# Optimization experiments

Measured on AMD Instinct MI355X. Metric: run time of the kernel, lower is better.

The kernel has to match this reference:

```python
import jax, jax.numpy as jnp
import numpy as np

B, S, D, H, HD, W, DFF = 2, 8192, 768, 12, 64, 256, 3072
NEG = -1e9


def ln(x, s, b, eps):
    m = jnp.mean(x, axis=-1, keepdims=True)
    v = jnp.mean((x - m) ** 2, axis=-1, keepdims=True)
    return (x - m) / jnp.sqrt(v + eps) * s + b


def band_attn(q, k, v, w):
    # q,k,v: [B,H,S,HD]; q already scaled by 1/sqrt(HD).
    b, h, s, d = q.shape
    nc = s // w  # non-overlapping query chunks of size w
    qc = q.reshape(b, h, nc, w, d)
    pad = ((0, 0), (0, 0), (w, w), (0, 0))
    kp = jnp.pad(k, pad)
    vp = jnp.pad(v, pad)
    # key chunk c covers global positions [c*w - w, c*w + 2w) -> length 3w
    idx = jnp.arange(nc)[:, None] * w + jnp.arange(3 * w)[None, :]  # [nc,3w]
    kc = kp[:, :, idx]  # [B,H,nc,3w,HD]
    vc = vp[:, :, idx]
    scores = jnp.einsum('bhcqd,bhckd->bhcqk', qc, kc)  # [B,H,nc,w,3w]
    # relative offset key-query: key global = c*w - w + j, query global = c*w + i
    rel = jnp.arange(3 * w)[None, :] - w - jnp.arange(w)[:, None]  # [w,3w]
    band = jnp.abs(rel) <= w
    kpos = jnp.arange(nc)[:, None] * w - w + jnp.arange(3 * w)[None, :]  # [nc,3w]
    valid = (kpos >= 0) & (kpos < s)
    mask = band[None, :, :] & valid[:, None, :]  # [nc,w,3w]
    scores = jnp.where(mask, scores, NEG)
    probs = jax.nn.softmax(scores, axis=-1)
    out = jnp.einsum('bhcqk,bhckd->bhcqd', probs, vc)
    return out.reshape(b, h, s, d)


def longformer_layer(hidden, pos_emb, tt_emb, emb_ln_s, emb_ln_b,
                     wq, bq, wk, bk, wv, bv, wo, bo, attn_ln_s, attn_ln_b,
                     wi, bi, wo2, bo2, out_ln_s, out_ln_b):
    # embeddings: inputs_embeds + position + token_type(0), LN eps 1e-12
    h = ln(hidden + pos_emb[None, :hidden.shape[1]] + tt_emb, emb_ln_s, emb_ln_b, 1e-12)
    def heads(x):
        return x.reshape(B, S, H, HD).transpose(0, 2, 1, 3)
    q = heads(h @ wq + bq) / jnp.sqrt(jnp.float32(HD))
    k = heads(h @ wk + bk)
    v = heads(h @ wv + bv)
    a = band_attn(q, k, v, W)  # [B,H,S,HD]
    a = a.transpose(0, 2, 1, 3).reshape(B, S, D)
    h2 = ln(h + (a @ wo + bo), attn_ln_s, attn_ln_b, 1e-12)
    inter = jax.nn.gelu(h2 @ wi + bi, approximate=False)
    return ln(h2 + (inter @ wo2 + bo2), out_ln_s, out_ln_b, 1e-12)


def setup_inputs() -> dict:
    key = jax.random.key(0)
    ks = jax.random.split(key, 16)
    wn = lambda k, shp: jax.random.normal(k, shp, jnp.float32) * 0.02
    d = {
        'src': jax.random.normal(ks[0], (B, S, D), jnp.float32),
        'pos_emb': wn(ks[1], (S, D)),
        'tt_emb': wn(ks[2], (D,)),
        'emb_ln_s': jnp.ones((D,)), 'emb_ln_b': jnp.zeros((D,)),
        'wq': wn(ks[3], (D, D)), 'bq': jnp.zeros((D,)),
        'wk': wn(ks[4], (D, D)), 'bk': jnp.zeros((D,)),
        'wv': wn(ks[5], (D, D)), 'bv': jnp.zeros((D,)),
        'wo': wn(ks[6], (D, D)), 'bo': jnp.zeros((D,)),
        'attn_ln_s': jnp.ones((D,)), 'attn_ln_b': jnp.zeros((D,)),
        'wi': wn(ks[7], (D, DFF)), 'bi': jnp.zeros((DFF,)),
        'wo2': wn(ks[8], (DFF, D)), 'bo2': jnp.zeros((D,)),
        'out_ln_s': jnp.ones((D,)), 'out_ln_b': jnp.zeros((D,)),
        'n1_s': jnp.ones((D,)), 'n1_b': jnp.zeros((D,)),
        'n2_s': jnp.ones((D,)), 'n2_b': jnp.zeros((D,)),
        'w1': wn(ks[9], (D, DFF)), 'b1': jnp.zeros((DFF,)),
        'w2': wn(ks[10], (DFF, D)), 'b2': jnp.zeros((D,)),
    }
    return d


def reference(src, pos_emb, tt_emb, emb_ln_s, emb_ln_b, wq, bq, wk, bk, wv, bv,
              wo, bo, attn_ln_s, attn_ln_b, wi, bi, wo2, bo2, out_ln_s, out_ln_b,
              n1_s, n1_b, n2_s, n2_b, w1, b1, w2, b2):
    hidden = ln(src, n1_s, n1_b, 1e-5)
    out = longformer_layer(hidden, pos_emb, tt_emb, emb_ln_s, emb_ln_b,
                           wq, bq, wk, bk, wv, bv, wo, bo, attn_ln_s, attn_ln_b,
                           wi, bi, wo2, bo2, out_ln_s, out_ln_b)
    src2 = src + out  # dropout is identity in eval
    ff = jax.nn.relu(ln(src2, n2_s, n2_b, 1e-5) @ w1 + b1)
    ff = ff @ w2 + b2
    return src2 + ff
```

## Files before the change

### kernel.cpp

```cpp
#include <hip/hip_runtime.h>

#define SLEN 8192
#define BD   768
#define NH   12
#define NTOK 16384
#define HTOK 8192

typedef __bf16 bf16;
typedef __bf16 bf16x8 __attribute__((ext_vector_type(8)));
typedef float  floatx4 __attribute__((ext_vector_type(4)));

#define MFMA16(a, b, c) __builtin_amdgcn_mfma_f32_16x16x32_bf16((a), (b), (c), 0, 0, 0)

__device__ __forceinline__ int iclamp(int v, int lo, int hi) {
  return v < lo ? lo : (v > hi ? hi : v);
}

__device__ __forceinline__ void gl2lds16(const bf16* g, bf16* l) {
  __builtin_amdgcn_global_load_lds(
      (const __attribute__((address_space(1))) void*)g,
      (__attribute__((address_space(3))) void*)l,
      16, 0, 0);
}

__global__ __launch_bounds__(256) void k_prep_w(const float* __restrict__ W,
                                                bf16* __restrict__ Wt,
                                                int K, int N, float scale) {
  __shared__ float tile[32][33];
  const int tid = threadIdx.x;
  const int tx = tid & 31, ty = tid >> 5;
  const int n0 = blockIdx.x * 32, k0 = blockIdx.y * 32;
#pragma unroll
  for (int i = 0; i < 32; i += 8)
    tile[ty + i][tx] = W[(size_t)(k0 + ty + i) * N + n0 + tx];
  __syncthreads();
#pragma unroll
  for (int i = 0; i < 32; i += 8)
    Wt[(size_t)(n0 + ty + i) * K + k0 + tx] = (bf16)(tile[tx][ty + i] * scale);
}

__global__ void k_prep_qkv_bias(const float* __restrict__ bq, const float* __restrict__ bk,
                                const float* __restrict__ bv, float* __restrict__ out) {
  int i = blockIdx.x * 256 + threadIdx.x;
  if (i < 768) out[i] = bq[i] * 0.125f;
  else if (i < 1536) out[i] = bk[i - 768];
  else if (i < 2304) out[i] = bv[i - 1536];
}

__device__ __forceinline__ float block_sum768(float v, float* red) {
#pragma unroll
  for (int off = 32; off > 0; off >>= 1) v += __shfl_down(v, off);
  __syncthreads();
  if ((threadIdx.x & 63) == 0) red[threadIdx.x >> 6] = v;
  __syncthreads();
  return red[0] + red[1] + red[2] + red[3];
}

__global__ __launch_bounds__(256) void k_ln_ln_emb(const float* __restrict__ src,
    const float* __restrict__ pos, const float* __restrict__ tt,
    const float* __restrict__ s1, const float* __restrict__ b1,
    const float* __restrict__ s2, const float* __restrict__ b2,
    float* __restrict__ hf, bf16* __restrict__ hb) {
  __shared__ float red[4];
  const int tid = threadIdx.x;
  const size_t row = blockIdx.x;
  const int sp = blockIdx.x & (SLEN - 1);
  const float* x = src + row * BD;
  float v0 = x[tid], v1 = x[tid + 256], v2 = x[tid + 512];
  const float mean = block_sum768(v0 + v1 + v2, red) * (1.f / 768.f);
  v0 -= mean; v1 -= mean; v2 -= mean;
  const float var = block_sum768(v0 * v0 + v1 * v1 + v2 * v2, red) * (1.f / 768.f);
  const float rstd = rsqrtf(var + 1e-5f);
  const float* pr = pos + (size_t)sp * BD;
  float y0 = v0 * rstd * s1[tid]       + b1[tid]       + pr[tid]       + tt[tid];
  float y1 = v1 * rstd * s1[tid + 256] + b1[tid + 256] + pr[tid + 256] + tt[tid + 256];
  float y2 = v2 * rstd * s1[tid + 512] + b1[tid + 512] + pr[tid + 512] + tt[tid + 512];
  const float mean2 = block_sum768(y0 + y1 + y2, red) * (1.f / 768.f);
  y0 -= mean2; y1 -= mean2; y2 -= mean2;
  const float var2 = block_sum768(y0 * y0 + y1 * y1 + y2 * y2, red) * (1.f / 768.f);
  const float rstd2 = rsqrtf(var2 + 1e-12f);
  float o0 = y0 * rstd2 * s2[tid]       + b2[tid];
  float o1 = y1 * rstd2 * s2[tid + 256] + b2[tid + 256];
  float o2 = y2 * rstd2 * s2[tid + 512] + b2[tid + 512];
  float* hr = hf + row * BD;
  bf16* hbr = hb + row * BD;
  hr[tid] = o0; hr[tid + 256] = o1; hr[tid + 512] = o2;
  hbr[tid] = (bf16)o0; hbr[tid + 256] = (bf16)o1; hbr[tid + 512] = (bf16)o2;
}

__global__ __launch_bounds__(256) void k_ln(const float* __restrict__ x,
    const float* __restrict__ s, const float* __restrict__ b, float eps,
    float* __restrict__ of, bf16* __restrict__ ob) {
  __shared__ float red[4];
  const int tid = threadIdx.x;
  const size_t row = blockIdx.x;
  const float* xr = x + row * BD;
  float v0 = xr[tid], v1 = xr[tid + 256], v2 = xr[tid + 512];
  const float mean = block_sum768(v0 + v1 + v2, red) * (1.f / 768.f);
  v0 -= mean; v1 -= mean; v2 -= mean;
  const float var = block_sum768(v0 * v0 + v1 * v1 + v2 * v2, red) * (1.f / 768.f);
  const float rstd = rsqrtf(var + eps);
  float o0 = v0 * rstd * s[tid] + b[tid];
  float o1 = v1 * rstd * s[tid + 256] + b[tid + 256];
  float o2 = v2 * rstd * s[tid + 512] + b[tid + 512];
  float* ofr = of + row * BD; bf16* obr = ob + row * BD;
  ofr[tid] = o0; ofr[tid + 256] = o1; ofr[tid + 512] = o2;
  obr[tid] = (bf16)o0; obr[tid + 256] = (bf16)o1; obr[tid + 512] = (bf16)o2;
}

__global__ __launch_bounds__(256) void k_ln_add_ln(const float* __restrict__ y,
    const float* __restrict__ src,
    const float* __restrict__ so, const float* __restrict__ bo_,
    const float* __restrict__ s2, const float* __restrict__ b2,
    float* __restrict__ src2, bf16* __restrict__ tb) {
  __shared__ float red[4];
  const int tid = threadIdx.x;
  const size_t row = blockIdx.x;
  const float* xr = y + row * BD;
  float v0 = xr[tid], v1 = xr[tid + 256], v2 = xr[tid + 512];
  const float mean = block_sum768(v0 + v1 + v2, red) * (1.f / 768.f);
  v0 -= mean; v1 -= mean; v2 -= mean;
  const float var = block_sum768(v0 * v0 + v1 * v1 + v2 * v2, red) * (1.f / 768.f);
  const float rstd = rsqrtf(var + 1e-12f);
  const float* sr = src + row * BD;
  float u0 = sr[tid]       + v0 * rstd * so[tid]       + bo_[tid];
  float u1 = sr[tid + 256] + v1 * rstd * so[tid + 256] + bo_[tid + 256];
  float u2 = sr[tid + 512] + v2 * rstd * so[tid + 512] + bo_[tid + 512];
  float* s2r = src2 + row * BD;
  s2r[tid] = u0; s2r[tid + 256] = u1; s2r[tid + 512] = u2;
  const float mean2 = block_sum768(u0 + u1 + u2, red) * (1.f / 768.f);
  u0 -= mean2; u1 -= mean2; u2 -= mean2;
  const float var2 = block_sum768(u0 * u0 + u1 * u1 + u2 * u2, red) * (1.f / 768.f);
  const float rstd2 = rsqrtf(var2 + 1e-5f);
  bf16* tr = tb + row * BD;
  tr[tid]       = (bf16)(u0 * rstd2 * s2[tid]       + b2[tid]);
  tr[tid + 256] = (bf16)(u1 * rstd2 * s2[tid + 256] + b2[tid + 256]);
  tr[tid + 512] = (bf16)(u2 * rstd2 * s2[tid + 512] + b2[tid + 512]);
}

template <int ACT, bool RES, bool OUTB>
__global__ __launch_bounds__(256, 2) void k_gemm(const bf16* __restrict__ A,
                                                 const bf16* __restrict__ Bt,
                                                 const float* __restrict__ bias,
                                                 const float* __restrict__ resid,
                                                 float* __restrict__ Cf,
                                                 bf16* __restrict__ Cb,
                                                 int M, int N, int K) {
  __shared__ __align__(16) bf16 As[128 * 32];
  __shared__ __align__(16) bf16 Bs[128 * 32];
  const int tid = threadIdx.x;
  const int lane = tid & 63, wave = tid >> 6;
  const int quad = lane >> 4, c = lane & 15;
  const int wr = wave >> 1, wc = wave & 1;
  const int n0 = blockIdx.x * 128, m0 = blockIdx.y * 128;

  const int rA0 = wave * 32 + (lane >> 2);
  const int rA1 = rA0 + 16;
  const int gch = (((lane & 3) ^ ((lane >> 3) & 3)) << 3);
  const bf16* gA0 = A  + (size_t)(m0 + rA0) * K + gch;
  const bf16* gA1 = A  + (size_t)(m0 + rA1) * K + gch;
  const bf16* gB0 = Bt + (size_t)(n0 + rA0) * K + gch;
  const bf16* gB1 = Bt + (size_t)(n0 + rA1) * K + gch;
  bf16* lA0 = As + wave * 1024;
  bf16* lA1 = As + wave * 1024 + 512;
  bf16* lB0 = Bs + wave * 1024;
  bf16* lB1 = Bs + wave * 1024 + 512;

  const int xorq = ((quad ^ ((c >> 1) & 3)) << 3);
  const bf16* aRd[4];
  const bf16* bRd[4];
#pragma unroll
  for (int i = 0; i < 4; ++i) {
    aRd[i] = As + (wr * 64 + i * 16 + c) * 32 + xorq;
    bRd[i] = Bs + (wc * 64 + i * 16 + c) * 32 + xorq;
  }

  floatx4 acc[4][4];
#pragma unroll
  for (int i = 0; i < 4; ++i)
#pragma unroll
    for (int j = 0; j < 4; ++j) acc[i][j] = floatx4{0.f, 0.f, 0.f, 0.f};

  for (int k0 = 0; k0 < K; k0 += 32) {
    __syncthreads();
    gl2lds16(gA0 + k0, lA0);
    gl2lds16(gA1 + k0, lA1);
    gl2lds16(gB0 + k0, lB0);
    gl2lds16(gB1 + k0, lB1);
    __syncthreads();
    bf16x8 af[4], bfv[4];
#pragma unroll
    for (int i = 0; i < 4; ++i) af[i] = *(const bf16x8*)aRd[i];
#pragma unroll
    for (int j = 0; j < 4; ++j) bfv[j] = *(const bf16x8*)bRd[j];
#pragma unroll
    for (int i = 0; i < 4; ++i)
#pragma unroll
      for (int j = 0; j < 4; ++j)
        acc[i][j] = MFMA16(af[i], bfv[j], acc[i][j]);
  }

  const int rbase = m0 + wr * 64 + quad * 4;
  const int cbase = n0 + wc * 64 + c;
#pragma unroll
  for (int i = 0; i < 4; ++i) {
#pragma unroll
    for (int j = 0; j < 4; ++j) {
      const int col = cbase + j * 16;
      const float bc = bias[col];
#pragma unroll
      for (int r = 0; r < 4; ++r) {
        const int row = rbase + i * 16 + r;
        float v = acc[i][j][r] + bc;
        if (RES) v += resid[(size_t)row * N + col];
        if (ACT == 1) v = 0.5f * v * (1.f + erff(v * 0.70710678118654752f));
        if (ACT == 2) v = fmaxf(v, 0.f);
        if (OUTB) Cb[(size_t)row * N + col] = (bf16)v;
        else      Cf[(size_t)row * N + col] = v;
      }
    }
  }
}

__global__ __launch_bounds__(256) void k_vtrans(const bf16* __restrict__ qkv_b, bf16* __restrict__ vt) {
  __shared__ bf16 tile[64][72];
  const int tid = threadIdx.x;
  const int blk = blockIdx.x;
  const int h  = blk >> 7;
  const int st = blk & 127;
  const int s0 = st * 64;
  {
    const int d = tid & 63, si4 = tid >> 6;
    const bf16* src = qkv_b + (size_t)s0 * 2304 + 1536 + h * 64 + d;
#pragma unroll
    for (int i = 0; i < 16; ++i) {
      int s = si4 * 16 + i;
      tile[s][d] = src[(size_t)s * 2304];
    }
  }
  __syncthreads();
  {
    const int s = tid & 63, di4 = tid >> 6;
#pragma unroll
    for (int i = 0; i < 16; ++i) {
      int d = di4 * 16 + i;
      vt[((size_t)(h * 64 + d)) * SLEN + s0 + s] = tile[s][d];
    }
  }
}

__global__ __launch_bounds__(256, 4) void k_attn(const bf16* __restrict__ qkv_b,
                                                 const bf16* __restrict__ vt,
                                                 bf16* __restrict__ aout_b) {
  __shared__ __align__(16) bf16 p_lds[4][640];
  const int tid  = threadIdx.x;
  const int wave = tid >> 6, lane = tid & 63;
  const int quad = lane >> 4, c = lane & 15;
  const int blk  = blockIdx.x;
  const int h    = blk >> 7;
  const int st   = blk & 127;
  const int q0   = st * 64 + wave * 16;

  const bf16* qp = qkv_b + (size_t)(q0 + c) * 2304 + h * 64 + quad * 8;
  bf16x8 aq0 = *(const bf16x8*)(qp);
  bf16x8 aq1 = *(const bf16x8*)(qp + 32);

  floatx4 o[4];
  float m[4], l[4];
#pragma unroll
  for (int r = 0; r < 4; ++r) {
    o[r] = floatx4{0.f, 0.f, 0.f, 0.f};
    m[r] = -1e30f; l[r] = 0.f;
  }
  bf16* plw = &p_lds[wave][0];

  for (int t = 0; t < 17; ++t) {
    const int kb = q0 - 256 + 32 * t;
    floatx4 s0 = floatx4{0.f, 0.f, 0.f, 0.f};
    floatx4 s1 = floatx4{0.f, 0.f, 0.f, 0.f};
    {
      const int kr0 = iclamp(kb + c, 0, SLEN - 1);
      const int kr1 = iclamp(kb + 16 + c, 0, SLEN - 1);
      const bf16* kp0 = qkv_b + (size_t)kr0 * 2304 + 768 + h * 64 + quad * 8;
      const bf16* kp1 = qkv_b + (size_t)kr1 * 2304 + 768 + h * 64 + quad * 8;
      bf16x8 k00 = *(const bf16x8*)(kp0);
      bf16x8 k01 = *(const bf16x8*)(kp0 + 32);
      bf16x8 k10 = *(const bf16x8*)(kp1);
      bf16x8 k11 = *(const bf16x8*)(kp1 + 32);
      s0 = MFMA16(aq0, k00, s0); s0 = MFMA16(aq1, k01, s0);
      s1 = MFMA16(aq0, k10, s1); s1 = MFMA16(aq1, k11, s1);
    }
    float tm[4];
#pragma unroll
    for (int r = 0; r < 4; ++r) {
      const int qpos = q0 + quad * 4 + r;
      const int k0p = kb + c, k1p = kb + 16 + c;
      int d0 = k0p - qpos; d0 = d0 < 0 ? -d0 : d0;
      int d1 = k1p - qpos; d1 = d1 < 0 ? -d1 : d1;
      if (!((unsigned)k0p < (unsigned)SLEN && d0 <= 256)) s0[r] = -INFINITY;
      if (!((unsigned)k1p < (unsigned)SLEN && d1 <= 256)) s1[r] = -INFINITY;
      tm[r] = fmaxf(s0[r], s1[r]);
    }
#pragma unroll
    for (int off = 1; off < 16; off <<= 1) {
#pragma unroll
      for (int r = 0; r < 4; ++r) tm[r] = fmaxf(tm[r], __shfl_xor(tm[r], off));
    }
    float rs[4];
#pragma unroll
    for (int r = 0; r < 4; ++r) {
      const float mn = fmaxf(m[r], tm[r]);
      const float al = __expf(m[r] - mn);
      m[r] = mn;
      s0[r] = __expf(s0[r] - mn);
      s1[r] = __expf(s1[r] - mn);
      rs[r] = s0[r] + s1[r];
      l[r] *= al;
#pragma unroll
      for (int n = 0; n < 4; ++n) o[n][r] *= al;
    }
#pragma unroll
    for (int off = 1; off < 16; off <<= 1) {
#pragma unroll
      for (int r = 0; r < 4; ++r) rs[r] += __shfl_xor(rs[r], off);
    }
#pragma unroll
    for (int r = 0; r < 4; ++r) {
      l[r] += rs[r];
      plw[(quad * 4 + r) * 40 + c]      = (bf16)s0[r];
      plw[(quad * 4 + r) * 40 + 16 + c] = (bf16)s1[r];
    }
    asm volatile("s_waitcnt lgkmcnt(0)" ::: "memory");
    bf16x8 pa = *(const bf16x8*)(plw + c * 40 + quad * 8);
    const int kvb = iclamp(kb + quad * 8, 0, SLEN - 8);
#pragma unroll
    for (int n = 0; n < 4; ++n) {
      const bf16* vp = vt + ((size_t)(h * 64 + n * 16 + c)) * SLEN + kvb;
      o[n] = MFMA16(pa, *(const bf16x8*)vp, o[n]);
    }
  }
#pragma unroll
  for (int r = 0; r < 4; ++r) {
    const float inv = 1.f / l[r];
    const size_t orow = (size_t)(q0 + quad * 4 + r) * BD + h * 64;
#pragma unroll
    for (int n = 0; n < 4; ++n)
      aout_b[orow + n * 16 + c] = (bf16)(o[n][r] * inv);
  }
}

extern "C" void kernel_launch(void* const* d_in, const int* in_sizes, int n_in,
                              void* d_out, int out_size, void* d_ws, size_t ws_size,
                              hipStream_t stream) {
  (void)in_sizes; (void)n_in; (void)out_size; (void)ws_size;
  const float* src     = (const float*)d_in[0];
  const float* pos_emb = (const float*)d_in[1];
  const float* tt_emb  = (const float*)d_in[2];
  const float* emb_s   = (const float*)d_in[3];
  const float* emb_b   = (const float*)d_in[4];
  const float* wq      = (const float*)d_in[5];
  const float* bq      = (const float*)d_in[6];
  const float* wk      = (const float*)d_in[7];
  const float* bk      = (const float*)d_in[8];
  const float* wv      = (const float*)d_in[9];
  const float* bv      = (const float*)d_in[10];
  const float* wo      = (const float*)d_in[11];
  const float* bo      = (const float*)d_in[12];
  const float* atn_s   = (const float*)d_in[13];
  const float* atn_b   = (const float*)d_in[14];
  const float* wi      = (const float*)d_in[15];
  const float* bi      = (const float*)d_in[16];
  const float* wo2     = (const float*)d_in[17];
  const float* bo2     = (const float*)d_in[18];
  const float* out_s   = (const float*)d_in[19];
  const float* out_b   = (const float*)d_in[20];
  const float* n1_s    = (const float*)d_in[21];
  const float* n1_b    = (const float*)d_in[22];
  const float* n2_s    = (const float*)d_in[23];
  const float* n2_b    = (const float*)d_in[24];
  const float* w1      = (const float*)d_in[25];
  const float* b1      = (const float*)d_in[26];
  const float* w2      = (const float*)d_in[27];
  const float* b2      = (const float*)d_in[28];

  char* ws = (char*)d_ws;
  size_t off = 0;
  auto alloc = [&](size_t bytes) {
    char* p = ws + off;
    off += (bytes + 255) & ~(size_t)255;
    return p;
  };

  bf16* qkvt  = (bf16*)alloc((size_t)2304 * 768 * 2);
  bf16* wot   = (bf16*)alloc((size_t)768 * 768 * 2);
  bf16* wit   = (bf16*)alloc((size_t)3072 * 768 * 2);
  bf16* wo2t  = (bf16*)alloc((size_t)768 * 3072 * 2);
  bf16* w1t   = (bf16*)alloc((size_t)3072 * 768 * 2);
  bf16* w2t   = (bf16*)alloc((size_t)768 * 3072 * 2);
  float* qkvb = (float*)alloc((size_t)2304 * 4);
  char* R1 = alloc((size_t)NTOK * BD * 4);
  char* R2 = alloc((size_t)NTOK * BD * 2);
  char* R3 = alloc((size_t)HTOK * 2304 * 2
                 + (size_t)NH * 64 * SLEN * 2
                 + (size_t)HTOK * BD * 2);

  float* h_f   = (float*)R1;
  bf16*  hb    = (bf16*)R2;
  bf16*  qkvB  = (bf16*)R3;
  bf16*  vtB   = (bf16*)(R3 + (size_t)HTOK * 2304 * 2);
  bf16*  aoutB = (bf16*)(R3 + (size_t)HTOK * 2304 * 2 + (size_t)NH * 64 * SLEN * 2);
  float* y1    = (float*)d_out;
  float* h2f   = (float*)R1;
  bf16*  h2b   = (bf16*)R2;
  bf16*  interC= (bf16*)R3;
  float* y2    = (float*)d_out;
  float* src2  = (float*)R1;
  bf16*  tb    = (bf16*)R2;
  bf16*  ff1C  = (bf16*)R3;
  float* outp  = (float*)d_out;

  dim3 blk(256);
  k_prep_w<<<dim3(24, 24), blk, 0, stream>>>(wq, qkvt,                 768, 768, 0.125f);
  k_prep_w<<<dim3(24, 24), blk, 0, stream>>>(wk, qkvt + 768 * 768,     768, 768, 1.f);
  k_prep_w<<<dim3(24, 24), blk, 0, stream>>>(wv, qkvt + 2 * 768 * 768, 768, 768, 1.f);
  k_prep_w<<<dim3(24, 24), blk, 0, stream>>>(wo, wot,                  768, 768, 1.f);
  k_prep_w<<<dim3(96, 24), blk, 0, stream>>>(wi, wit,    768, 3072, 1.f);
  k_prep_w<<<dim3(24, 96), blk, 0, stream>>>(wo2, wo2t, 3072, 768,  1.f);
  k_prep_w<<<dim3(96, 24), blk, 0, stream>>>(w1, w1t,    768, 3072, 1.f);
  k_prep_w<<<dim3(24, 96), blk, 0, stream>>>(w2, w2t,   3072, 768,  1.f);
  k_prep_qkv_bias<<<dim3(9), blk, 0, stream>>>(bq, bk, bv, qkvb);

  k_ln_ln_emb<<<dim3(NTOK), blk, 0, stream>>>(src, pos_emb, tt_emb, n1_s, n1_b,
                                              emb_s, emb_b, h_f, hb);
  for (int b = 0; b < 2; ++b) {
    const size_t tok0 = (size_t)b * HTOK;
    k_gemm<0, false, true><<<dim3(18, 64), blk, 0, stream>>>(
        hb + tok0 * BD, qkvt, qkvb, nullptr, nullptr, qkvB, HTOK, 2304, 768);
    k_vtrans<<<dim3(NH * 128), blk, 0, stream>>>(qkvB, vtB);
    k_attn<<<dim3(NH * 128), blk, 0, stream>>>(qkvB, vtB, aoutB);
    k_gemm<0, true, false><<<dim3(6, 64), blk, 0, stream>>>(
        aoutB, wot, bo, h_f + tok0 * BD, y1 + tok0 * BD, nullptr, HTOK, 768, 768);
  }
  k_ln<<<dim3(NTOK), blk, 0, stream>>>(y1, atn_s, atn_b, 1e-12f, h2f, h2b);
  for (int cchunk = 0; cchunk < 2; ++cchunk) {
    const size_t tok0 = (size_t)cchunk * HTOK;
    k_gemm<1, false, true><<<dim3(24, 64), blk, 0, stream>>>(
        h2b + tok0 * BD, wit, bi, nullptr, nullptr, interC, HTOK, 3072, 768);
    k_gemm<0, true, false><<<dim3(6, 64), blk, 0, stream>>>(
        interC, wo2t, bo2, h2f + tok0 * BD, y2 + tok0 * BD, nullptr, HTOK, 768, 3072);
  }
  k_ln_add_ln<<<dim3(NTOK), blk, 0, stream>>>(y2, src, out_s, out_b, n2_s, n2_b, src2, tb);
  for (int cchunk = 0; cchunk < 2; ++cchunk) {
    const size_t tok0 = (size_t)cchunk * HTOK;
    k_gemm<2, false, true><<<dim3(24, 64), blk, 0, stream>>>(
        tb + tok0 * BD, w1t, b1, nullptr, nullptr, ff1C, HTOK, 3072, 768);
    k_gemm<0, true, false><<<dim3(6, 64), blk, 0, stream>>>(
        ff1C, w2t, b2, src2 + tok0 * BD, outp + tok0 * BD, nullptr, HTOK, 768, 3072);
  }
}
```

Before: 1.193 ms.

## Stage K/V tiles in LDS with double-buffered async loads in band attention

The band-attention kernel now loads shared 64-key K and V tiles into LDS once per workgroup, using double-buffered global_load_lds with an XOR swizzle. Before, each wave read K and V straight from global memory with its own loads. Key blocks are now 64 wide, and blocks fully outside the sequence are skipped through per-tile loop bounds. The band mask is applied only on the two edge tiles. The block index is also remapped so neighbouring workgroups spread across XCDs, which adds __syncthreads per tile and more LDS use, lowering occupancy headroom.

```diff
diff --git a/kernel.cpp b/kernel.cpp
--- a/kernel.cpp
+++ b/kernel.cpp
@@ -252,18 +252,29 @@
 __global__ __launch_bounds__(256, 4) void k_attn(const bf16* __restrict__ qkv_b,
                                                  const bf16* __restrict__ vt,
                                                  bf16* __restrict__ aout_b) {
-  __shared__ __align__(16) bf16 p_lds[4][640];
+  __shared__ __align__(16) bf16 Ks[2][64 * 64];
+  __shared__ __align__(16) bf16 Vs[2][64 * 64];
+  __shared__ __align__(16) bf16 Ps[4][16 * 64];
   const int tid  = threadIdx.x;
   const int wave = tid >> 6, lane = tid & 63;
   const int quad = lane >> 4, c = lane & 15;
-  const int blk  = blockIdx.x;
-  const int h    = blk >> 7;
-  const int st   = blk & 127;
-  const int q0   = st * 64 + wave * 16;
+  const int blk0 = blockIdx.x;
+  const int wg   = ((blk0 & 7) * 192) + (blk0 >> 3);
+  const int h    = wg >> 7;
+  const int st   = wg & 127;
+  const int q0b  = st * 64;
+  const int q0   = q0b + wave * 16;
 
   const bf16* qp = qkv_b + (size_t)(q0 + c) * 2304 + h * 64 + quad * 8;
-  bf16x8 aq0 = *(const bf16x8*)(qp);
-  bf16x8 aq1 = *(const bf16x8*)(qp + 32);
+  const bf16x8 aq0 = *(const bf16x8*)(qp);
+  const bf16x8 aq1 = *(const bf16x8*)(qp + 32);
+
+  const int srow  = lane >> 3;
+  const int chunk = ((lane & 7) ^ srow) << 3;
+  const int krow0 = wave * 16 + srow;
+
+  const int xlo = (quad ^ (c & 7)) << 3;
+  const int xhi = ((quad + 4) ^ (c & 7)) << 3;
 
   floatx4 o[4];
   float m[4], l[4];
@@ -272,73 +283,99 @@
     o[r] = floatx4{0.f, 0.f, 0.f, 0.f};
     m[r] = -1e30f; l[r] = 0.f;
   }
-  bf16* plw = &p_lds[wave][0];
-
-  for (int t = 0; t < 17; ++t) {
-    const int kb = q0 - 256 + 32 * t;
-    floatx4 s0 = floatx4{0.f, 0.f, 0.f, 0.f};
-    floatx4 s1 = floatx4{0.f, 0.f, 0.f, 0.f};
-    {
-      const int kr0 = iclamp(kb + c, 0, SLEN - 1);
-      const int kr1 = iclamp(kb + 16 + c, 0, SLEN - 1);
-      const bf16* kp0 = qkv_b + (size_t)kr0 * 2304 + 768 + h * 64 + quad * 8;
-      const bf16* kp1 = qkv_b + (size_t)kr1 * 2304 + 768 + h * 64 + quad * 8;
-      bf16x8 k00 = *(const bf16x8*)(kp0);
-      bf16x8 k01 = *(const bf16x8*)(kp0 + 32);
-      bf16x8 k10 = *(const bf16x8*)(kp1);
-      bf16x8 k11 = *(const bf16x8*)(kp1 + 32);
-      s0 = MFMA16(aq0, k00, s0); s0 = MFMA16(aq1, k01, s0);
-      s1 = MFMA16(aq0, k10, s1); s1 = MFMA16(aq1, k11, s1);
-    }
-    float tm[4];
-#pragma unroll
-    for (int r = 0; r < 4; ++r) {
-      const int qpos = q0 + quad * 4 + r;
-      const int k0p = kb + c, k1p = kb + 16 + c;
-      int d0 = k0p - qpos; d0 = d0 < 0 ? -d0 : d0;
-      int d1 = k1p - qpos; d1 = d1 < 0 ? -d1 : d1;
-      if (!((unsigned)k0p < (unsigned)SLEN && d0 <= 256)) s0[r] = -INFINITY;
-      if (!((unsigned)k1p < (unsigned)SLEN && d1 <= 256)) s1[r] = -INFINITY;
-      tm[r] = fmaxf(s0[r], s1[r]);
-    }
-#pragma unroll
-    for (int off = 1; off < 16; off <<= 1) {
+  bf16* Pw = &Ps[wave][0];
+
+  const int t_lo = st < 4 ? 4 - st : 0;
+  const int t_hi = st > 123 ? 132 - st : 9;
+
+  auto stage = [&](int buf, int t) {
+    const int kb  = q0b - 256 + 64 * t;
+    const int kr0 = iclamp(kb + krow0, 0, SLEN - 1);
+    const int kr1 = iclamp(kb + krow0 + 8, 0, SLEN - 1);
+    gl2lds16(qkv_b + (size_t)kr0 * 2304 + 768 + h * 64 + chunk, &Ks[buf][wave * 1024]);
+    gl2lds16(qkv_b + (size_t)kr1 * 2304 + 768 + h * 64 + chunk, &Ks[buf][wave * 1024 + 512]);
+    const int kbc = iclamp(kb, 0, SLEN - 64);
+    gl2lds16(vt + (size_t)(h * 64 + krow0) * SLEN + kbc + chunk, &Vs[buf][wave * 1024]);
+    gl2lds16(vt + (size_t)(h * 64 + krow0 + 8) * SLEN + kbc + chunk, &Vs[buf][wave * 1024 + 512]);
+  };
+
+  int cur = 0;
+  stage(0, t_lo);
+  for (int t = t_lo; t < t_hi; ++t) {
+    __syncthreads();
+    if (t + 1 < t_hi) stage(cur ^ 1, t + 1);
+    const int kb = q0b - 256 + 64 * t;
+    const bf16* Kb = &Ks[cur][0];
+    const bf16* Vb = &Vs[cur][0];
+
+    floatx4 s[4];
+#pragma unroll
+    for (int i = 0; i < 4; ++i) s[i] = floatx4{0.f, 0.f, 0.f, 0.f};
+#pragma unroll
+    for (int ks = 0; ks < 4; ++ks) {
+      const bf16* kr = Kb + (ks * 16 + c) * 64;
+      s[ks] = MFMA16(aq0, *(const bf16x8*)(kr + xlo), s[ks]);
+      s[ks] = MFMA16(aq1, *(const bf16x8*)(kr + xhi), s[ks]);
+    }
+    if (t == 0 || t == 8) {
+#pragma unroll
+      for (int ks = 0; ks < 4; ++ks)
+#pragma unroll
+        for (int r = 0; r < 4; ++r) {
+          int d = (kb + ks * 16 + c) - (q0 + quad * 4 + r);
+          d = d < 0 ? -d : d;
+          if (d > 256) s[ks][r] = -INFINITY;
+        }
+    }
+
+    float tm[4], rs[4];
+#pragma unroll
+    for (int r = 0; r < 4; ++r)
+      tm[r] = fmaxf(fmaxf(s[0][r], s[1][r]), fmaxf(s[2][r], s[3][r]));
+#pragma unroll
+    for (int off = 1; off < 16; off <<= 1)
 #pragma unroll
       for (int r = 0; r < 4; ++r) tm[r] = fmaxf(tm[r], __shfl_xor(tm[r], off));
-    }
-    float rs[4];
 #pragma unroll
     for (int r = 0; r < 4; ++r) {
       const float mn = fmaxf(m[r], tm[r]);
       const float al = __expf(m[r] - mn);
       m[r] = mn;
-      s0[r] = __expf(s0[r] - mn);
-      s1[r] = __expf(s1[r] - mn);
-      rs[r] = s0[r] + s1[r];
+      float sum = 0.f;
+#pragma unroll
+      for (int ks = 0; ks < 4; ++ks) { s[ks][r] = __expf(s[ks][r] - mn); sum += s[ks][r]; }
+      rs[r] = sum;
       l[r] *= al;
 #pragma unroll
       for (int n = 0; n < 4; ++n) o[n][r] *= al;
     }
 #pragma unroll
-    for (int off = 1; off < 16; off <<= 1) {
+    for (int off = 1; off < 16; off <<= 1)
 #pragma unroll
       for (int r = 0; r < 4; ++r) rs[r] += __shfl_xor(rs[r], off);
-    }
-#pragma unroll
-    for (int r = 0; r < 4; ++r) {
-      l[r] += rs[r];
-      plw[(quad * 4 + r) * 40 + c]      = (bf16)s0[r];
-      plw[(quad * 4 + r) * 40 + 16 + c] = (bf16)s1[r];
-    }
+#pragma unroll
+    for (int r = 0; r < 4; ++r) l[r] += rs[r];
+
+#pragma unroll
+    for (int ks = 0; ks < 4; ++ks)
+#pragma unroll
+      for (int r = 0; r < 4; ++r) {
+        const int prow = quad * 4 + r;
+        const int col  = ks * 16 + c;
+        Pw[prow * 64 + ((((col >> 3) ^ (prow & 7)) << 3) | (col & 7))] = (bf16)s[ks][r];
+      }
     asm volatile("s_waitcnt lgkmcnt(0)" ::: "memory");
-    bf16x8 pa = *(const bf16x8*)(plw + c * 40 + quad * 8);
-    const int kvb = iclamp(kb + quad * 8, 0, SLEN - 8);
+    const bf16x8 pa0 = *(const bf16x8*)(Pw + c * 64 + xlo);
+    const bf16x8 pa1 = *(const bf16x8*)(Pw + c * 64 + xhi);
 #pragma unroll
     for (int n = 0; n < 4; ++n) {
-      const bf16* vp = vt + ((size_t)(h * 64 + n * 16 + c)) * SLEN + kvb;
-      o[n] = MFMA16(pa, *(const bf16x8*)vp, o[n]);
-    }
-  }
+      const bf16* vr = Vb + (n * 16 + c) * 64;
+      o[n] = MFMA16(pa0, *(const bf16x8*)(vr + xlo), o[n]);
+      o[n] = MFMA16(pa1, *(const bf16x8*)(vr + xhi), o[n]);
+    }
+    cur ^= 1;
+  }
+
 #pragma unroll
   for (int r = 0; r < 4; ++r) {
     const float inv = 1.f / l[r];
```

Measured after the change: 1.076 ms. -9.8%, faster.
